# Kernel optimization log

Measured on AMD Instinct MI355X. Metric: run time of the kernel, lower is better.

Reference implementation:

```python
import jax, jax.numpy as jnp
import numpy as np

N_NODES = 100000
N_EDGES = 1600000
DIM = 128


def setup_inputs() -> dict:
    key = jax.random.key(0)
    k_x, k_e, k_wm, k_bm, k_wu, k_bu = jax.random.split(key, 6)
    bound = 1.0 / np.sqrt(DIM)
    return {
        "x": jax.random.normal(k_x, (N_NODES, DIM), dtype=jnp.float32),
        "edge_index": jax.random.randint(k_e, (2, N_EDGES), 0, N_NODES, dtype=jnp.int64),
        "W_msg": jax.random.uniform(k_wm, (DIM, DIM), jnp.float32, -bound, bound),
        "b_msg": jax.random.uniform(k_bm, (DIM,), jnp.float32, -bound, bound),
        "W_upd": jax.random.uniform(k_wu, (DIM, DIM), jnp.float32, -bound, bound),
        "b_upd": jax.random.uniform(k_bu, (DIM,), jnp.float32, -bound, bound),
    }


def reference(x, edge_index, W_msg, b_msg, W_upd, b_upd):
    # message_net: Linear + ReLU on all nodes  [N, D]
    messages = jax.nn.relu(x @ W_msg.T + b_msg)
    src, dst = edge_index[0], edge_index[1]
    # gather by src, scatter-add by dst (index_add)  [N, D]
    aggregated = jax.ops.segment_sum(messages[src], dst, num_segments=x.shape[0])
    # update_net: Linear + ReLU, then residual
    updated = jax.nn.relu(aggregated @ W_upd.T + b_upd)
    return updated + x
```

## Files before the change

kernel.cpp:

```cpp
#include <hip/hip_runtime.h>
#include <hip/hip_bf16.h>

#define DIM 128
#define BNODES 64
#define CNODES 1024
#define NCMAX 128
#define NBMAX 2048
#define CCAP 20480
#define BCAP 2048
#define FB 16

typedef __attribute__((ext_vector_type(8))) short bf16x8;
typedef __attribute__((ext_vector_type(4))) float f32x4;

__device__ inline ushort f2bf(float f) {
    uint u = __float_as_uint(f);
    u += 0x7fffu + ((u >> 16) & 1u);
    return (ushort)(u >> 16);
}
__device__ inline uint pack2(float lo, float hi) {
    return (uint)f2bf(lo) | ((uint)f2bf(hi) << 16);
}

template<bool RESID, bool BF16OUT>
__device__ __forceinline__
void linear_body(const float* in, const float* __restrict__ W,
                 const float* __restrict__ b, const float* __restrict__ xres,
                 void* outv, int n_tiles, int bid, int nblocks, uint4* Wl)
{
    const int t = threadIdx.x;
    for (int q = t; q < 2048; q += 256) {
        const int j = q >> 4, c = q & 15;
        const float4 lo = ((const float4*)(W + j * 128 + c * 8))[0];
        const float4 hi = ((const float4*)(W + j * 128 + c * 8))[1];
        uint4 pk;
        pk.x = pack2(lo.x, lo.y); pk.y = pack2(lo.z, lo.w);
        pk.z = pack2(hi.x, hi.y); pk.w = pack2(hi.z, hi.w);
        Wl[j * 16 + (c ^ (j & 15))] = pk;
    }
    __syncthreads();

    const int lane = t & 63;
    const int lo4 = lane & 15;
    const int g   = lane >> 4;

    float bias[8];
    #pragma unroll
    for (int ct = 0; ct < 8; ++ct) bias[ct] = b[ct * 16 + lo4];

    const int wid = (bid * 256 + t) >> 6;
    const int nw  = (nblocks * 256) >> 6;

    for (int tile = wid; tile < n_tiles; tile += nw) {
        const int arow = tile * 16 + lo4;
        const float4* ap = (const float4*)(in + (size_t)arow * DIM + g * 32);
        float4 v[8];
        #pragma unroll
        for (int i = 0; i < 8; ++i) v[i] = ap[i];

        bf16x8 afrag[4];
        #pragma unroll
        for (int ks = 0; ks < 4; ++ks) {
            union { bf16x8 v8; uint u[4]; } a;
            a.u[0] = pack2(v[2*ks].x,   v[2*ks].y);
            a.u[1] = pack2(v[2*ks].z,   v[2*ks].w);
            a.u[2] = pack2(v[2*ks+1].x, v[2*ks+1].y);
            a.u[3] = pack2(v[2*ks+1].z, v[2*ks+1].w);
            afrag[ks] = a.v8;
        }

        f32x4 acc[8];
        #pragma unroll
        for (int ct = 0; ct < 8; ++ct)
            acc[ct] = (f32x4){bias[ct], bias[ct], bias[ct], bias[ct]};

        #pragma unroll
        for (int ks = 0; ks < 4; ++ks) {
            #pragma unroll
            for (int ct = 0; ct < 8; ++ct) {
                const int jrow = ct * 16 + lo4;
                const bf16x8 bfrag = *((const bf16x8*)&Wl[jrow * 16 + ((g * 4 + ks) ^ lo4)]);
                acc[ct] = __builtin_amdgcn_mfma_f32_16x16x32_bf16(afrag[ks], bfrag, acc[ct], 0, 0, 0);
            }
        }

        #pragma unroll
        for (int ct = 0; ct < 8; ++ct) {
            #pragma unroll
            for (int r = 0; r < 4; ++r) {
                const int orow = tile * 16 + g * 4 + r;
                const int ocol = ct * 16 + lo4;
                float val = fmaxf(acc[ct][r], 0.f);
                if constexpr (RESID) val += xres[(size_t)orow * DIM + ocol];
                if constexpr (BF16OUT)
                    ((ushort*)outv)[(size_t)orow * DIM + ocol] = f2bf(val);
                else
                    ((float*)outv)[(size_t)orow * DIM + ocol] = val;
            }
        }
    }
}

__global__ __launch_bounds__(256, 2)
void lin1_coarse_kernel(const float* x, const float* __restrict__ Wm,
                        const float* __restrict__ bm, ushort* msg, int n_tiles,
                        const int* __restrict__ ei, int* __restrict__ ccur,
                        uint* __restrict__ cedges, int n_edges, int ncb, int cblocks)
{
    __shared__ uint4 Wl[128 * 16];
    __shared__ int histL[NCMAX];
    __shared__ int curL[NCMAX];

    if ((int)blockIdx.x < cblocks) {
        const int t = threadIdx.x;
        if (t < ncb) histL[t] = 0;
        __syncthreads();
        const int chunk = (n_edges + cblocks - 1) / cblocks;
        const int e0 = blockIdx.x * chunk;
        const int e1 = min(e0 + chunk, n_edges);
        for (int e = e0 + t; e < e1; e += 256)
            atomicAdd(&histL[ei[n_edges + e] >> 10], 1);
        __syncthreads();
        if (t < ncb)
            curL[t] = histL[t] ? atomicAdd(&ccur[t], histL[t]) : 0;
        __syncthreads();
        for (int e = e0 + t; e < e1; e += 256) {
            const int src = ei[e];
            const int dst = ei[n_edges + e];
            const int c = dst >> 10;
            const int pos = atomicAdd(&curL[c], 1);
            if (pos < CCAP)
                cedges[(size_t)c * CCAP + pos] = ((uint)src << 10) | (uint)(dst & 1023);
        }
    } else {
        linear_body<false, true>(x, Wm, bm, nullptr, msg, n_tiles,
                                 (int)blockIdx.x - cblocks, (int)gridDim.x - cblocks, Wl);
    }
}

__global__ __launch_bounds__(256, 2)
void lin2_kernel(const float* agg, const float* __restrict__ Wu,
                 const float* __restrict__ bu, const float* __restrict__ x,
                 float* out, int n_tiles)
{
    __shared__ uint4 Wl[128 * 16];
    linear_body<true, false>(agg, Wu, bu, x, out, n_tiles,
                             (int)blockIdx.x, (int)gridDim.x, Wl);
}

__global__ __launch_bounds__(256)
void fine_scatter_kernel(const int* __restrict__ ccnt, const uint* __restrict__ cedges,
                         int* __restrict__ gcur, uint* __restrict__ bedges, int ncb)
{
    __shared__ int histL[FB];
    __shared__ int curL[FB];
    const int t = threadIdx.x;
    const int c = blockIdx.x >> 3;
    const int s = blockIdx.x & 7;
    const int cnt = min(ccnt[c], CCAP);
    const int chunk = (cnt + 7) / 8;
    const int e0 = s * chunk;
    const int e1 = min(e0 + chunk, cnt);
    if (t < FB) histL[t] = 0;
    __syncthreads();
    const uint* ce = cedges + (size_t)c * CCAP;
    for (int i = e0 + t; i < e1; i += 256)
        atomicAdd(&histL[(ce[i] & 1023u) >> 6], 1);
    __syncthreads();
    if (t < FB)
        curL[t] = histL[t] ? atomicAdd(&gcur[c * FB + t], histL[t]) : 0;
    __syncthreads();
    for (int i = e0 + t; i < e1; i += 256) {
        const uint p = ce[i];
        const uint dl = p & 1023u;
        const int f = (int)(dl >> 6);
        const int pos = atomicAdd(&curL[f], 1);
        if (pos < BCAP)
            bedges[(size_t)(c * FB + f) * BCAP + pos] = ((p >> 10) << 6) | (dl & 63u);
    }
}

__global__ __launch_bounds__(512)
void bucket_gather_kernel(const uint* __restrict__ msg, const int* __restrict__ gcur,
                          const uint* __restrict__ bedges, float* __restrict__ agg,
                          int n_nodes)
{
    __shared__ uint edgesL[BCAP];
    __shared__ int  srcL[BCAP];
    __shared__ int histL[BNODES];
    __shared__ int inclL[BNODES];
    __shared__ int cursL[BNODES];

    const int t = threadIdx.x;
    const int b = blockIdx.x;
    const int cnt = min(gcur[b], BCAP);
    const uint* be = bedges + (size_t)b * BCAP;

    if (t < BNODES) histL[t] = 0;
    __syncthreads();
    for (int i = t; i < cnt; i += 512) {
        const uint p = be[i];
        edgesL[i] = p;
        atomicAdd(&histL[p & 63u], 1);
    }
    __syncthreads();
    if (t < BNODES) inclL[t] = histL[t];
    for (int off = 1; off < BNODES; off <<= 1) {
        int add = 0;
        __syncthreads();
        if (t < BNODES && t >= off) add = inclL[t - off];
        __syncthreads();
        if (t < BNODES) inclL[t] += add;
    }
    __syncthreads();
    if (t < BNODES) cursL[t] = inclL[t] - histL[t];
    __syncthreads();
    for (int i = t; i < cnt; i += 512) {
        const uint p = edgesL[i];
        const int pos = atomicAdd(&cursL[p & 63u], 1);
        srcL[pos] = (int)(p >> 6);
    }
    __syncthreads();

    const int lane = t & 63;
    const int w = t >> 6;
    for (int dl = w; dl < BNODES; dl += 8) {
        const int node = b * BNODES + dl;
        if (node >= n_nodes) break;
        const int e1 = inclL[dl];
        const int e0 = e1 - histL[dl];
        float a0 = 0.f, a1 = 0.f;
        int i = e0;
        for (; i + 4 <= e1; i += 4) {
            const int sA = srcL[i + 0], sB = srcL[i + 1];
            const int sC = srcL[i + 2], sD = srcL[i + 3];
            const uint mA = msg[(size_t)sA * 64 + lane];
            const uint mB = msg[(size_t)sB * 64 + lane];
            const uint mC = msg[(size_t)sC * 64 + lane];
            const uint mD = msg[(size_t)sD * 64 + lane];
            a0 += __uint_as_float(mA << 16) + __uint_as_float(mB << 16)
                + __uint_as_float(mC << 16) + __uint_as_float(mD << 16);
            a1 += __uint_as_float(mA & 0xffff0000u) + __uint_as_float(mB & 0xffff0000u)
                + __uint_as_float(mC & 0xffff0000u) + __uint_as_float(mD & 0xffff0000u);
        }
        for (; i < e1; ++i) {
            const uint m = msg[(size_t)srcL[i] * 64 + lane];
            a0 += __uint_as_float(m << 16);
            a1 += __uint_as_float(m & 0xffff0000u);
        }
        ((float2*)(agg + (size_t)node * DIM))[lane] = make_float2(a0, a1);
    }
}

extern "C" void kernel_launch(void* const* d_in, const int* in_sizes, int n_in,
                              void* d_out, int out_size, void* d_ws, size_t ws_size,
                              hipStream_t stream)
{
    const float* x  = (const float*)d_in[0];
    const int*   ei = (const int*)d_in[1];
    const float* Wm = (const float*)d_in[2];
    const float* bm = (const float*)d_in[3];
    const float* Wu = (const float*)d_in[4];
    const float* bu = (const float*)d_in[5];

    const int N = in_sizes[0] / DIM;
    const int E = in_sizes[1] / 2;
    const int nb  = (N + BNODES - 1) / BNODES;
    const int ncb = (N + CNODES - 1) / CNODES;

    char* ws = (char*)d_ws;
    ushort* msg = (ushort*)ws;
    size_t o = (size_t)N * DIM * sizeof(ushort);
    int* ccur = (int*)(ws + o); o += (size_t)NCMAX * 4;
    int* gcur = (int*)(ws + o); o += (size_t)NBMAX * 4;
    o = (o + 255) & ~(size_t)255;
    uint* cedges = (uint*)(ws + o); o += (size_t)ncb * CCAP * 4;
    o = (o + 255) & ~(size_t)255;
    uint* bedges = (uint*)(ws + o);

    float* out = (float*)d_out;
    float* agg = out;

    const int n_tiles = N / 16;

    hipMemsetAsync(ccur, 0, (size_t)(NCMAX + NBMAX) * 4, stream);

    lin1_coarse_kernel<<<2048, 256, 0, stream>>>(x, Wm, bm, msg, n_tiles,
                                                 ei, ccur, cedges, E, ncb, 1024);

    fine_scatter_kernel<<<ncb * 8, 256, 0, stream>>>(ccur, cedges, gcur, bedges, ncb);

    bucket_gather_kernel<<<nb, 512, 0, stream>>>((const uint*)msg, gcur, bedges, agg, N);

    lin2_kernel<<<1024, 256, 0, stream>>>(agg, Wu, bu, x, out, n_tiles);
}
```

Before: 157.7 us.

## Fuse update linear into gather kernel and prepack update weights in lin1 launch

Removes the separate lin2 kernel. Each gather block now keeps its 64 aggregated rows in shared memory as swizzled bf16 and runs the update MFMA, ReLU and residual itself, so the fp32 aggregate never makes a round trip through global memory. Eight extra blocks in the first kernel prepack W_upd into swizzled bf16 for the gather blocks to copy into LDS. The cost is much more shared memory per gather block (about 56KB), which may lower occupancy for the latency-bound gather.

```diff
diff --git a/kernel.cpp b/kernel.cpp
--- a/kernel.cpp
+++ b/kernel.cpp
@@ -22,11 +22,11 @@
     return (uint)f2bf(lo) | ((uint)f2bf(hi) << 16);
 }
 
-template<bool RESID, bool BF16OUT>
+template<bool BF16OUT>
 __device__ __forceinline__
 void linear_body(const float* in, const float* __restrict__ W,
-                 const float* __restrict__ b, const float* __restrict__ xres,
-                 void* outv, int n_tiles, int bid, int nblocks, uint4* Wl)
+                 const float* __restrict__ b, void* outv, int n_tiles,
+                 int bid, int nblocks, uint4* Wl)
 {
     const int t = threadIdx.x;
     for (int q = t; q < 2048; q += 256) {
@@ -91,7 +91,6 @@
                 const int orow = tile * 16 + g * 4 + r;
                 const int ocol = ct * 16 + lo4;
                 float val = fmaxf(acc[ct][r], 0.f);
-                if constexpr (RESID) val += xres[(size_t)orow * DIM + ocol];
                 if constexpr (BF16OUT)
                     ((ushort*)outv)[(size_t)orow * DIM + ocol] = f2bf(val);
                 else
@@ -105,18 +104,21 @@
 void lin1_coarse_kernel(const float* x, const float* __restrict__ Wm,
                         const float* __restrict__ bm, ushort* msg, int n_tiles,
                         const int* __restrict__ ei, int* __restrict__ ccur,
-                        uint* __restrict__ cedges, int n_edges, int ncb, int cblocks)
+                        uint* __restrict__ cedges, int n_edges, int ncb,
+                        const float* __restrict__ Wu, uint4* __restrict__ wupk,
+                        int cb, int lb)
 {
     __shared__ uint4 Wl[128 * 16];
     __shared__ int histL[NCMAX];
     __shared__ int curL[NCMAX];
 
-    if ((int)blockIdx.x < cblocks) {
+    const int bid = (int)blockIdx.x;
+    if (bid < cb) {
         const int t = threadIdx.x;
         if (t < ncb) histL[t] = 0;
         __syncthreads();
-        const int chunk = (n_edges + cblocks - 1) / cblocks;
-        const int e0 = blockIdx.x * chunk;
+        const int chunk = (n_edges + cb - 1) / cb;
+        const int e0 = bid * chunk;
         const int e1 = min(e0 + chunk, n_edges);
         for (int e = e0 + t; e < e1; e += 256)
             atomicAdd(&histL[ei[n_edges + e] >> 10], 1);
@@ -132,20 +134,18 @@
             if (pos < CCAP)
                 cedges[(size_t)c * CCAP + pos] = ((uint)src << 10) | (uint)(dst & 1023);
         }
+    } else if (bid < cb + lb) {
+        linear_body<true>(x, Wm, bm, msg, n_tiles, bid - cb, lb, Wl);
     } else {
-        linear_body<false, true>(x, Wm, bm, nullptr, msg, n_tiles,
-                                 (int)blockIdx.x - cblocks, (int)gridDim.x - cblocks, Wl);
-    }
-}
-
-__global__ __launch_bounds__(256, 2)
-void lin2_kernel(const float* agg, const float* __restrict__ Wu,
-                 const float* __restrict__ bu, const float* __restrict__ x,
-                 float* out, int n_tiles)
-{
-    __shared__ uint4 Wl[128 * 16];
-    linear_body<true, false>(agg, Wu, bu, x, out, n_tiles,
-                             (int)blockIdx.x, (int)gridDim.x, Wl);
+        const int q = (bid - cb - lb) * 256 + (int)threadIdx.x;
+        const int j = q >> 4, c = q & 15;
+        const float4 lo = ((const float4*)(Wu + j * 128 + c * 8))[0];
+        const float4 hi = ((const float4*)(Wu + j * 128 + c * 8))[1];
+        uint4 pk;
+        pk.x = pack2(lo.x, lo.y); pk.y = pack2(lo.z, lo.w);
+        pk.z = pack2(hi.x, hi.y); pk.w = pack2(hi.z, hi.w);
+        wupk[j * 16 + (c ^ (j & 15))] = pk;
+    }
 }
 
 __global__ __launch_bounds__(256)
@@ -181,12 +181,15 @@
 }
 
 __global__ __launch_bounds__(512)
-void bucket_gather_kernel(const uint* __restrict__ msg, const int* __restrict__ gcur,
-                          const uint* __restrict__ bedges, float* __restrict__ agg,
-                          int n_nodes)
-{
-    __shared__ uint edgesL[BCAP];
-    __shared__ int  srcL[BCAP];
+void gather_lin2_kernel(const uint* __restrict__ msg, const int* __restrict__ gcur,
+                        const uint* __restrict__ bedges, const uint4* __restrict__ wupk,
+                        const float* __restrict__ bu, const float* __restrict__ x,
+                        float* __restrict__ out, int n_nodes)
+{
+    __shared__ uint4 Wl[128 * 16];
+    __shared__ uint  aggL[BNODES * 64];
+    __shared__ uint  edgesL[BCAP];
+    __shared__ int   srcL[BCAP];
     __shared__ int histL[BNODES];
     __shared__ int inclL[BNODES];
     __shared__ int cursL[BNODES];
@@ -196,6 +199,8 @@
     const int cnt = min(gcur[b], BCAP);
     const uint* be = bedges + (size_t)b * BCAP;
 
+    for (int q = t; q < 2048; q += 512) Wl[q] = wupk[q];
+
     if (t < BNODES) histL[t] = 0;
     __syncthreads();
     for (int i = t; i < cnt; i += 512) {
@@ -224,6 +229,7 @@
 
     const int lane = t & 63;
     const int w = t >> 6;
+
     for (int dl = w; dl < BNODES; dl += 8) {
         const int node = b * BNODES + dl;
         if (node >= n_nodes) break;
@@ -248,7 +254,54 @@
             a0 += __uint_as_float(m << 16);
             a1 += __uint_as_float(m & 0xffff0000u);
         }
-        ((float2*)(agg + (size_t)node * DIM))[lane] = make_float2(a0, a1);
+        aggL[dl * 64 + ((((lane >> 2) ^ (dl & 15)) << 2) | (lane & 3))] = pack2(a0, a1);
+    }
+    __syncthreads();
+
+    const int lo4 = lane & 15;
+    const int g   = lane >> 4;
+    const int tw  = w & 3;
+    const int ch  = w >> 2;
+
+    float bias[4];
+    #pragma unroll
+    for (int ct = 0; ct < 4; ++ct) bias[ct] = bu[(ch * 4 + ct) * 16 + lo4];
+
+    const int arow = tw * 16 + lo4;
+    bf16x8 afrag[4];
+    #pragma unroll
+    for (int ks = 0; ks < 4; ++ks) {
+        const int cidx = (g * 4 + ks) ^ (arow & 15);
+        afrag[ks] = *(const bf16x8*)&aggL[arow * 64 + cidx * 4];
+    }
+
+    f32x4 acc[4];
+    #pragma unroll
+    for (int ct = 0; ct < 4; ++ct)
+        acc[ct] = (f32x4){bias[ct], bias[ct], bias[ct], bias[ct]};
+
+    #pragma unroll
+    for (int ks = 0; ks < 4; ++ks) {
+        #pragma unroll
+        for (int ct = 0; ct < 4; ++ct) {
+            const int jrow = (ch * 4 + ct) * 16 + lo4;
+            const bf16x8 bfrag = *((const bf16x8*)&Wl[jrow * 16 + ((g * 4 + ks) ^ lo4)]);
+            acc[ct] = __builtin_amdgcn_mfma_f32_16x16x32_bf16(afrag[ks], bfrag, acc[ct], 0, 0, 0);
+        }
+    }
+
+    const int node0 = b * BNODES;
+    #pragma unroll
+    for (int ct = 0; ct < 4; ++ct) {
+        #pragma unroll
+        for (int r = 0; r < 4; ++r) {
+            const int orow = node0 + tw * 16 + g * 4 + r;
+            const int ocol = (ch * 4 + ct) * 16 + lo4;
+            if (orow < n_nodes) {
+                const float val = fmaxf(acc[ct][r], 0.f) + x[(size_t)orow * DIM + ocol];
+                out[(size_t)orow * DIM + ocol] = val;
+            }
+        }
     }
 }
 
@@ -274,23 +327,23 @@
     int* ccur = (int*)(ws + o); o += (size_t)NCMAX * 4;
     int* gcur = (int*)(ws + o); o += (size_t)NBMAX * 4;
     o = (o + 255) & ~(size_t)255;
+    uint4* wupk = (uint4*)(ws + o); o += 2048 * sizeof(uint4);
+    o = (o + 255) & ~(size_t)255;
     uint* cedges = (uint*)(ws + o); o += (size_t)ncb * CCAP * 4;
     o = (o + 255) & ~(size_t)255;
     uint* bedges = (uint*)(ws + o);
 
     float* out = (float*)d_out;
-    float* agg = out;
-
     const int n_tiles = N / 16;
 
     hipMemsetAsync(ccur, 0, (size_t)(NCMAX + NBMAX) * 4, stream);
 
-    lin1_coarse_kernel<<<2048, 256, 0, stream>>>(x, Wm, bm, msg, n_tiles,
-                                                 ei, ccur, cedges, E, ncb, 1024);
+    lin1_coarse_kernel<<<2056, 256, 0, stream>>>(x, Wm, bm, msg, n_tiles,
+                                                 ei, ccur, cedges, E, ncb,
+                                                 Wu, wupk, 1024, 1024);
 
     fine_scatter_kernel<<<ncb * 8, 256, 0, stream>>>(ccur, cedges, gcur, bedges, ncb);
 
-    bucket_gather_kernel<<<nb, 512, 0, stream>>>((const uint*)msg, gcur, bedges, agg, N);
-
-    lin2_kernel<<<1024, 256, 0, stream>>>(agg, Wu, bu, x, out, n_tiles);
-}
+    gather_lin2_kernel<<<nb, 512, 0, stream>>>((const uint*)msg, gcur, bedges,
+                                               (const uint4*)wupk, bu, x, out, N);
+}
```

Result: slower. 176.6 us (+12.0%).
